# Performance work log

Hardware: AMD Instinct MI355X
Metric: run time of the kernel (lower is better)

## Reference

```python
import jax, jax.numpy as jnp
import numpy as np

N, E, FEAT, DIM, B = 200000, 1600000, 128, 64, 256


def setup_inputs() -> dict:
    key = jax.random.key(0)
    ks = jax.random.split(key, 16)
    s = 0.05
    x = jax.random.normal(ks[0], (N, FEAT), jnp.float32)
    edge_index = jax.random.randint(ks[1], (2, E), 0, N)
    batch = jnp.sort(jax.random.randint(ks[2], (N,), 0, B))
    return {
        'x': x,
        'edge_index': edge_index,
        'batch': batch,
        'lin0_w': jax.random.normal(ks[3], (FEAT, DIM), jnp.float32) * s,
        'lin0_b': jax.random.normal(ks[4], (DIM,), jnp.float32) * s,
        'conv_w': jax.random.normal(ks[5], (DIM, DIM), jnp.float32) * s,
        'conv_b': jax.random.normal(ks[6], (DIM,), jnp.float32) * s,
        'gru_w_ih': jax.random.normal(ks[7], (3 * DIM, DIM), jnp.float32) * s,
        'gru_w_hh': jax.random.normal(ks[8], (3 * DIM, DIM), jnp.float32) * s,
        'gru_b_ih': jax.random.normal(ks[9], (3 * DIM,), jnp.float32) * s,
        'gru_b_hh': jax.random.normal(ks[10], (3 * DIM,), jnp.float32) * s,
        'lstm_w_ih': jax.random.normal(ks[11], (4 * DIM, 2 * DIM), jnp.float32) * s,
        'lstm_w_hh': jax.random.normal(ks[12], (4 * DIM, DIM), jnp.float32) * s,
        'lstm_b_ih': jax.random.normal(ks[13], (4 * DIM,), jnp.float32) * s,
        'lstm_b_hh': jax.random.normal(ks[14], (4 * DIM,), jnp.float32) * s,
    }


def reference(x, edge_index, batch, lin0_w, lin0_b, conv_w, conv_b,
              gru_w_ih, gru_w_hh, gru_b_ih, gru_b_hh,
              lstm_w_ih, lstm_w_hh, lstm_b_ih, lstm_b_hh):
    n = x.shape[0]
    d = lin0_w.shape[1]
    # --- GCN normalization with self-loops (PyG gcn_norm, symmetric) ---
    loops = jnp.arange(n)
    row = jnp.concatenate([edge_index[0], loops])  # source nodes
    col = jnp.concatenate([edge_index[1], loops])  # target nodes
    deg = jax.ops.segment_sum(jnp.ones(row.shape, jnp.float32), col, num_segments=N)
    dinv = jnp.where(deg > 0, jax.lax.rsqrt(deg), 0.0)
    norm = dinv[row] * dinv[col]  # [E+N]

    out = jax.nn.relu(x @ lin0_w + lin0_b)  # [N, D]
    h = out  # GRU hidden (layer dim squeezed)
    feat = out
    for _ in range(3):
        # GCNConv: aggregate normalized neighbor messages
        hw = out @ conv_w                                   # [N, D]
        m = jax.ops.segment_sum(norm[:, None] * hw[row], col, num_segments=N) + conv_b
        m = jax.nn.relu(m)
        # torch.nn.GRU cell (gate order: reset, update, new)
        gi = m @ gru_w_ih.T + gru_b_ih
        gh = h @ gru_w_hh.T + gru_b_hh
        ir, iz, in_ = jnp.split(gi, 3, axis=-1)
        hr, hz, hn = jnp.split(gh, 3, axis=-1)
        r = jax.nn.sigmoid(ir + hr)
        z = jax.nn.sigmoid(iz + hz)
        ncand = jnp.tanh(in_ + r * hn)
        h = (1.0 - z) * ncand + z * h
        out = h
        feat = out

    # --- Set2Set pooling, processing_steps=3 (LSTM: 2D -> D) ---
    q_star = jnp.zeros((B, 2 * d), x.dtype)
    hl = jnp.zeros((B, d), x.dtype)
    cl = jnp.zeros((B, d), x.dtype)
    for _ in range(3):
        gates = q_star @ lstm_w_ih.T + lstm_b_ih + hl @ lstm_w_hh.T + lstm_b_hh
        i_, f_, g_, o_ = jnp.split(gates, 4, axis=-1)  # torch order i,f,g,o
        cl = jax.nn.sigmoid(f_) * cl + jax.nn.sigmoid(i_) * jnp.tanh(g_)
        hl = jax.nn.sigmoid(o_) * jnp.tanh(cl)
        q = hl                                             # [B, D]
        e = jnp.sum(out * q[batch], axis=-1)               # [N]
        emax = jax.ops.segment_max(e, batch, num_segments=B)
        a = jnp.exp(e - jax.lax.stop_gradient(emax)[batch])
        denom = jax.ops.segment_sum(a, batch, num_segments=B)
        a = a / denom[batch]                               # scatter-softmax
        r_read = jax.ops.segment_sum(a[:, None] * out, batch, num_segments=B)
        q_star = jnp.concatenate([q, r_read], axis=-1)     # [B, 2D]
    return (q_star, feat)
```

## Files before the change

### kernel.cpp

```cpp
#include <hip/hip_runtime.h>
#include <math.h>

#define FEATD 128
#define DIM 64
#define NB 256
#define SCB 256
#define KB 16
#define RNG 128
#define NBUCKMAX 2048
#define CH1 8192

typedef short bf16x8 __attribute__((ext_vector_type(8)));
typedef float f32x4 __attribute__((ext_vector_type(4)));

__device__ __forceinline__ float frcp_(float x){ return __builtin_amdgcn_rcpf(x); }
__device__ __forceinline__ float sigmoidf_(float x){ return frcp_(1.f+__expf(-x)); }
__device__ __forceinline__ float tanhf_(float x){ float e=__expf(2.f*x); return 1.f-2.f*frcp_(e+1.f); }

__device__ __forceinline__ unsigned short f2bf(float f){
  unsigned u = __float_as_uint(f);
  unsigned r = (u + 0x7FFFu + ((u>>16)&1u)) >> 16;
  return (unsigned short)r;
}
__device__ __forceinline__ float bf2f(unsigned short s){
  return __uint_as_float(((unsigned)s)<<16);
}

__device__ __forceinline__ int lower_bound_i(const int* __restrict__ a, int n, int key){
  int lo=0, hi=n;
  while(lo<hi){ int mid=(lo+hi)>>1; if(a[mid]<key) lo=mid+1; else hi=mid; }
  return lo;
}

__global__ void k_count(const int* __restrict__ col, int* __restrict__ deg, int E){
  int i=blockIdx.x*blockDim.x+threadIdx.x;
  if(i<E) atomicAdd(&deg[col[i]],1);
}

__global__ void k_dinv(const int* __restrict__ deg, float* __restrict__ dinv, int n){
  int i=blockIdx.x*blockDim.x+threadIdx.x;
  if(i<n) dinv[i]=rsqrtf((float)(deg[i]+1));
}

__global__ __launch_bounds__(256) void k_scan_part(const int* __restrict__ deg, int* __restrict__ part, int n){
  __shared__ int s[256];
  int b=blockIdx.x;
  int chunk=(n+SCB-1)/SCB;
  int lo=b*chunk, hi=min(lo+chunk,n);
  int acc=0;
  for(int i=lo+threadIdx.x;i<hi;i+=256) acc+=deg[i];
  s[threadIdx.x]=acc; __syncthreads();
  for(int off=128;off;off>>=1){
    if(threadIdx.x<off) s[threadIdx.x]+=s[threadIdx.x+off];
    __syncthreads();
  }
  if(threadIdx.x==0) part[b]=s[0];
}

__global__ __launch_bounds__(256) void k_scan_mid(int* __restrict__ part){
  __shared__ int s[256];
  int t=threadIdx.x;
  s[t]=part[t]; __syncthreads();
  for(int off=1;off<256;off<<=1){
    int v=(t>=off)? s[t-off]:0;
    __syncthreads();
    s[t]+=v;
    __syncthreads();
  }
  part[t]=(t>0)? s[t-1]:0;
}

__global__ __launch_bounds__(256) void k_scan_out(const int* __restrict__ deg, const int* __restrict__ part,
                                                  int* __restrict__ rp, int* __restrict__ gcur, int n){
  __shared__ int s[256];
  int b=blockIdx.x, t=threadIdx.x;
  int chunk=(n+SCB-1)/SCB;
  int lo=b*chunk, hi=min(lo+chunk,n);
  int tchunk=(chunk+255)/256;
  int tlo=lo+t*tchunk, thi=min(tlo+tchunk,hi);
  int acc=0;
  for(int i=tlo;i<thi;i++) acc+=deg[i];
  s[t]=acc; __syncthreads();
  for(int off=1;off<256;off<<=1){
    int v=(t>=off)? s[t-off]:0;
    __syncthreads();
    s[t]+=v;
    __syncthreads();
  }
  int pre=part[b]+((t>0)? s[t-1]:0);
  for(int i=tlo;i<thi;i++){
    rp[i]=pre;
    if((i&(RNG-1))==0) gcur[(i>>7)*32]=pre;
    pre+=deg[i];
  }
  if(b==SCB-1 && t==0) rp[n]=part[b]+s[255];
}

__global__ __launch_bounds__(256) void k_binscat(const int* __restrict__ row, const int* __restrict__ col,
                       int* __restrict__ gcur, unsigned* __restrict__ tmp, int E, int nbuck){
  __shared__ int lcnt[NBUCKMAX];
  __shared__ int lcur[NBUCKMAX];
  int t=threadIdx.x;
  for(int i=t;i<nbuck;i+=256) lcnt[i]=0;
  __syncthreads();
  int lo=blockIdx.x*CH1, hi=min(lo+CH1,E);
  for(int i=lo+t;i<hi;i+=256) atomicAdd(&lcnt[col[i]>>7],1);
  __syncthreads();
  for(int i=t;i<nbuck;i+=256){
    int cnt=lcnt[i];
    lcur[i]=(cnt>0)? atomicAdd(&gcur[i*32],cnt):0;
  }
  __syncthreads();
  for(int i=lo+t;i<hi;i+=256){
    int c=col[i], r=row[i];
    int pos=atomicAdd(&lcur[c>>7],1);
    tmp[pos]=((unsigned)r<<7)|(unsigned)(c&127);
  }
}

__global__ __launch_bounds__(256) void k_place(const unsigned* __restrict__ tmp, const int* __restrict__ rp,
                      const float* __restrict__ dinv, int2* __restrict__ epack, int n, int nbuck){
  __shared__ int lfill[RNG];
  __shared__ int lrp[RNG];
  __shared__ float ldv[RNG];
  int b=blockIdx.x, t=threadIdx.x;
  int nbase=b*RNG;
  int nn=min(RNG,n-nbase);
  if(t<nn){ lfill[t]=0; lrp[t]=rp[nbase+t]; ldv[t]=dinv[nbase+t]; }
  __syncthreads();
  int lo=rp[nbase], hi=rp[min(nbase+RNG,n)];
  for(int j=lo+t;j<hi;j+=256){
    unsigned v=tmp[j];
    int cl=v&127;
    int r=(int)(v>>7);
    int pos=atomicAdd(&lfill[cl],1);
    epack[lrp[cl]+pos]=make_int2(r,__float_as_int(dinv[r]*ldv[cl]));
  }
}

__global__ void k_prep_plain(const float* __restrict__ W, unsigned short* __restrict__ Bf, int K, int C){
  int i=blockIdx.x*blockDim.x+threadIdx.x;
  if(i>=K*C) return;
  int k=i/C, c=i%C;
  int t=c>>4, s=k>>5, lane=(c&15)|(((k>>3)&3)<<4), r=k&7;
  int S=K>>5;
  Bf[(((t*S)+s)*64+lane)*8+r]=f2bf(W[(size_t)k*C+c]);
}

__global__ void k_prep_gru(const float* __restrict__ wih, const float* __restrict__ whh,
                           unsigned short* __restrict__ Bf){
  int i=blockIdx.x*blockDim.x+threadIdx.x;
  if(i>=128*256) return;
  int k=i>>8, c=i&255;
  float v;
  if(c<128){
    v = (k<64) ? wih[c*64+k] : whh[c*64+(k-64)];
  } else if(c<192){
    v = (k<64) ? wih[c*64+k] : 0.f;
  } else {
    v = (k<64) ? 0.f : whh[(c-64)*64+(k-64)];
  }
  int t=c>>4, s=k>>5, lane=(c&15)|(((k>>3)&3)<<4), r=k&7;
  Bf[(((s*16)+t)*64+lane)*8+r]=f2bf(v);
}

__global__ __launch_bounds__(256) void k_lin0(const float* __restrict__ x, const unsigned short* __restrict__ Bf,
                      const float* __restrict__ bias,
                      unsigned short* __restrict__ hb, int ngrp){
  int l=threadIdx.x&63;
  int g=blockIdx.x*4+(threadIdx.x>>6);
  if(g>=ngrp) return;
  int row16=l&15, koff=(l>>4)*8;
  f32x4 acc[4]={};
  const float* xr = x + (size_t)(g*16+row16)*128 + koff;
  #pragma unroll
  for(int s=0;s<4;s++){
    f32x4 a0=*(const f32x4*)(xr+s*32);
    f32x4 a1=*(const f32x4*)(xr+s*32+4);
    bf16x8 af;
    #pragma unroll
    for(int r=0;r<4;r++){ af[r]=(short)f2bf(a0[r]); af[4+r]=(short)f2bf(a1[r]); }
    #pragma unroll
    for(int t=0;t<4;t++){
      bf16x8 bf=*(const bf16x8*)(Bf+(((t*4)+s)*64+l)*8);
      acc[t]=__builtin_amdgcn_mfma_f32_16x16x32_bf16(af,bf,acc[t],0,0,0);
    }
  }
  int rbase=g*16+(l>>4)*4;
  #pragma unroll
  for(int t=0;t<4;t++){
    int c=t*16+(l&15);
    float b=bias[c];
    #pragma unroll
    for(int j=0;j<4;j++){
      int node=rbase+j;
      float v=fmaxf(acc[t][j]+b,0.f);
      hb[(size_t)node*64+c]=f2bf(v);
    }
  }
}

__global__ __launch_bounds__(256) void k_aggregate(const unsigned short* __restrict__ hb, const int* __restrict__ rp,
                        const int2* __restrict__ epack, const float* __restrict__ dinv,
                        unsigned short* __restrict__ aggb, int n){
  int node=blockIdx.x*4+(threadIdx.x>>6);
  int lane=threadIdx.x&63;
  if(node>=n) return;
  int q=lane>>4, l16=lane&15;
  const uint2* hb64=(const uint2*)hb;
  float a0=0.f,a1=0.f,a2=0.f,a3=0.f, b0=0.f,b1=0.f,b2=0.f,b3=0.f;
  int s=rp[node], e=rp[node+1];
  int j=s+q;
  for(; j+4<e; j+=8){
    int2 e0=epack[j];
    int2 e1=epack[j+4];
    uint2 p0=hb64[((unsigned)e0.x<<4)+l16];
    uint2 p1=hb64[((unsigned)e1.x<<4)+l16];
    float n0=__int_as_float(e0.y), n1=__int_as_float(e1.y);
    a0+=n0*bf2f((unsigned short)p0.x);
    a1+=n0*bf2f((unsigned short)(p0.x>>16));
    a2+=n0*bf2f((unsigned short)p0.y);
    a3+=n0*bf2f((unsigned short)(p0.y>>16));
    b0+=n1*bf2f((unsigned short)p1.x);
    b1+=n1*bf2f((unsigned short)(p1.x>>16));
    b2+=n1*bf2f((unsigned short)p1.y);
    b3+=n1*bf2f((unsigned short)(p1.y>>16));
  }
  for(; j<e; j+=4){
    int2 e0=epack[j];
    uint2 p0=hb64[((unsigned)e0.x<<4)+l16];
    float n0=__int_as_float(e0.y);
    a0+=n0*bf2f((unsigned short)p0.x);
    a1+=n0*bf2f((unsigned short)(p0.x>>16));
    a2+=n0*bf2f((unsigned short)p0.y);
    a3+=n0*bf2f((unsigned short)(p0.y>>16));
  }
  a0+=b0; a1+=b1; a2+=b2; a3+=b3;
  if(q==0){
    float dv=dinv[node]; dv*=dv;
    uint2 ps=hb64[((unsigned)node<<4)+l16];
    a0+=dv*bf2f((unsigned short)ps.x);
    a1+=dv*bf2f((unsigned short)(ps.x>>16));
    a2+=dv*bf2f((unsigned short)ps.y);
    a3+=dv*bf2f((unsigned short)(ps.y>>16));
  }
  a0+=__shfl_xor(a0,16); a0+=__shfl_xor(a0,32);
  a1+=__shfl_xor(a1,16); a1+=__shfl_xor(a1,32);
  a2+=__shfl_xor(a2,16); a2+=__shfl_xor(a2,32);
  a3+=__shfl_xor(a3,16); a3+=__shfl_xor(a3,32);
  if(q==0){
    uint2 outp;
    outp.x=(unsigned)f2bf(a0)|(((unsigned)f2bf(a1))<<16);
    outp.y=(unsigned)f2bf(a2)|(((unsigned)f2bf(a3))<<16);
    ((uint2*)aggb)[((unsigned)node<<4)+l16]=outp;
  }
}

__global__ __launch_bounds__(256) void k_gru(const unsigned short* __restrict__ aggb, unsigned short* hb,
                     const unsigned short* __restrict__ Bcnv, const float* __restrict__ cb,
                     const unsigned short* __restrict__ Bgru,
                     const float* __restrict__ bih, const float* __restrict__ bhh,
                     float* h, int last, int ngrp, int n){
  __shared__ __align__(16) unsigned short Bs[16384];
  __shared__ __align__(16) unsigned short Bc[4096];
  __shared__ __align__(16) unsigned short mt[4][16][72];
  int tid=threadIdx.x;
  int l=tid&63, w=tid>>6;
  int g=blockIdx.x*4+w;
  bool act = g<ngrp;
  int gc = act? g : (ngrp-1);
  int row16=l&15, koff=(l>>4)*8;
  int node_r=gc*16+row16;
  int rbase=gc*16+(l>>4)*4;

  const unsigned short* ar = aggb + (size_t)node_r*64 + koff;
  const unsigned short* hr = hb   + (size_t)node_r*64 + koff;
  bf16x8 a_agg0=*(const bf16x8*)(ar);
  bf16x8 a_agg1=*(const bf16x8*)(ar+32);
  bf16x8 a_h0=*(const bf16x8*)(hr);
  bf16x8 a_h1=*(const bf16x8*)(hr+32);
  float hold[16];
  #pragma unroll
  for(int t=0;t<4;t++)
    #pragma unroll
    for(int j=0;j<4;j++)
      hold[t*4+j]=bf2f(hb[(size_t)(rbase+j)*64 + t*16+(l&15)]);

  {
    const f32x4* gs=(const f32x4*)Bcnv; f32x4* ls=(f32x4*)Bc;
    #pragma unroll
    for(int i=0;i<2;i++) ls[i*256+tid]=gs[i*256+tid];
    const f32x4* gh=(const f32x4*)Bgru; f32x4* lh=(f32x4*)Bs;
    #pragma unroll
    for(int i=0;i<8;i++) lh[i*256+tid]=gh[i*256+tid];
  }
  __syncthreads();

  f32x4 accm[4]={};
  #pragma unroll
  for(int s=0;s<2;s++){
    bf16x8 af=(s==0)? a_agg0:a_agg1;
    #pragma unroll
    for(int t=0;t<4;t++){
      bf16x8 bf=*(const bf16x8*)(Bc+((t*2+s)*64+l)*8);
      accm[t]=__builtin_amdgcn_mfma_f32_16x16x32_bf16(af,bf,accm[t],0,0,0);
    }
  }
  #pragma unroll
  for(int t=0;t<4;t++){
    int c=t*16+(l&15);
    float b=cb[c];
    #pragma unroll
    for(int j=0;j<4;j++)
      mt[w][(l>>4)*4+j][c]=f2bf(fmaxf(accm[t][j]+b,0.f));
  }

  f32x4 acc[16]={};
  #pragma unroll
  for(int s=0;s<2;s++){
    bf16x8 af=*(const bf16x8*)&mt[w][row16][koff+s*32];
    #pragma unroll
    for(int t=0;t<16;t++){
      bf16x8 bf=*(const bf16x8*)(Bs+((s*16+t)*64+l)*8);
      acc[t]=__builtin_amdgcn_mfma_f32_16x16x32_bf16(af,bf,acc[t],0,0,0);
    }
  }
  __syncthreads();
  {
    const f32x4* gh=(const f32x4*)(Bgru+16384); f32x4* lh=(f32x4*)Bs;
    #pragma unroll
    for(int i=0;i<8;i++) lh[i*256+tid]=gh[i*256+tid];
  }
  __syncthreads();

  #pragma unroll
  for(int s=0;s<2;s++){
    bf16x8 af=(s==0)? a_h0:a_h1;
    #pragma unroll
    for(int t=0;t<16;t++){
      bf16x8 bf=*(const bf16x8*)(Bs+((s*16+t)*64+l)*8);
      acc[t]=__builtin_amdgcn_mfma_f32_16x16x32_bf16(af,bf,acc[t],0,0,0);
    }
  }

  if(!act) return;
  #pragma unroll
  for(int t=0;t<4;t++){
    int d=t*16+(l&15);
    float br =bih[d]    +bhh[d];
    float bz =bih[64+d] +bhh[64+d];
    float bni=bih[128+d];
    float bnh=bhh[128+d];
    #pragma unroll
    for(int j=0;j<4;j++){
      int node=rbase+j;
      if(node<n){
        float r  = sigmoidf_(acc[t][j]   + br);
        float z  = sigmoidf_(acc[4+t][j] + bz);
        float nc = tanhf_(acc[8+t][j] + bni + r*(acc[12+t][j] + bnh));
        float hn = (1.f-z)*nc + z*hold[t*4+j];
        if(last) h[(size_t)node*64+d]=hn;
        hb[(size_t)node*64+d]=f2bf(hn);
      }
    }
  }
}

__global__ __launch_bounds__(256) void k_attn_part(const unsigned short* __restrict__ hb, const int* __restrict__ batch,
                        const float* __restrict__ hl, float* __restrict__ apart, int n){
  int b=blockIdx.x/KB, kb=blockIdx.x%KB;
  int tid=threadIdx.x, lane=tid&63, w=tid>>6;
  __shared__ float qs[64];
  __shared__ float wm[4], wsm[4];
  __shared__ float wacc[4][64];
  if(tid<64) qs[tid]=hl[b*64+tid];
  int lo=lower_bound_i(batch,n,b), hi=lower_bound_i(batch,n,b+1);
  int cnt=hi-lo;
  int chunk=(cnt+KB-1)/KB;
  int slo=lo+kb*chunk, shi=min(slo+chunk,hi);
  __syncthreads();
  float q=qs[lane];
  float mw=-3.0e38f, sw=0.f, aw=0.f;
  for(int i=slo+w;i<shi;i+=4){
    float f=bf2f(hb[(size_t)i*64+lane]);
    float v=f*q;
    #pragma unroll
    for(int off=32;off;off>>=1) v+=__shfl_xor(v,off);
    if(v>mw){
      float sc=__expf(mw-v);
      sw=sw*sc+1.f;
      aw=aw*sc+f;
      mw=v;
    } else {
      float p=__expf(v-mw);
      sw+=p;
      aw+=p*f;
    }
  }
  if(lane==0){ wm[w]=mw; wsm[w]=sw; }
  wacc[w][lane]=aw;
  __syncthreads();
  if(w==0){
    float M=fmaxf(fmaxf(wm[0],wm[1]),fmaxf(wm[2],wm[3]));
    float S=0.f, A=0.f;
    #pragma unroll
    for(int k=0;k<4;k++){
      float sc=__expf(wm[k]-M);
      S+=wsm[k]*sc;
      A+=wacc[k][lane]*sc;
    }
    float* p=apart+(size_t)blockIdx.x*68;
    p[lane]=A;
    if(lane==0){ p[64]=M; p[65]=S; }
  }
}

__global__ __launch_bounds__(256) void k_merge_lstm(const float* __restrict__ apart,
                   float* __restrict__ qstar, float* __restrict__ hl, float* __restrict__ cl,
                   const float* __restrict__ wih, const float* __restrict__ whh,
                   const float* __restrict__ bih, const float* __restrict__ bhh,
                   int do_merge, int do_lstm){
  int b=blockIdx.x, tid=threadIdx.x;
  __shared__ float qs[128];
  __shared__ float gates[256];
  if(do_merge){
    if(tid<64){
      const float* p0=apart+(size_t)b*KB*68;
      float M=-3.0e38f;
      #pragma unroll
      for(int k=0;k<KB;k++) M=fmaxf(M,p0[k*68+64]);
      float S=0.f, A=0.f;
      #pragma unroll
      for(int k=0;k<KB;k++){
        float sc=__expf(p0[k*68+64]-M);
        S+=p0[k*68+65]*sc;
        A+=p0[k*68+tid]*sc;
      }
      float inv=(S>0.f)? 1.f/S:0.f;
      float r=A*inv;
      qs[64+tid]=r;
      qstar[b*128+64+tid]=r;
    }
  } else {
    if(tid<64) qs[64+tid]=qstar[b*128+64+tid];
  }
  if(tid<64) qs[tid]=hl[b*64+tid];
  __syncthreads();
  if(!do_lstm) return;
  float acc=bih[tid]+bhh[tid];
  const float* wi=wih+(size_t)tid*128;
  #pragma unroll 8
  for(int k=0;k<128;k++) acc+=qs[k]*wi[k];
  const float* w2=whh+(size_t)tid*64;
  #pragma unroll 8
  for(int k=0;k<64;k++) acc+=qs[k]*w2[k];
  gates[tid]=acc;
  __syncthreads();
  if(tid<64){
    float i_=gates[tid], f_=gates[64+tid], g_=gates[128+tid], o_=gates[192+tid];
    float c=sigmoidf_(f_)*cl[b*64+tid]+sigmoidf_(i_)*tanhf(g_);
    float hn=sigmoidf_(o_)*tanhf(c);
    cl[b*64+tid]=c; hl[b*64+tid]=hn;
    qstar[b*128+tid]=hn;
  }
}

extern "C" void kernel_launch(void* const* d_in, const int* in_sizes, int n_in,
                              void* d_out, int out_size, void* d_ws, size_t ws_size,
                              hipStream_t stream){
  const float* x      =(const float*)d_in[0];
  const int*   ei     =(const int*)d_in[1];
  const int*   batch  =(const int*)d_in[2];
  const float* lin0_w =(const float*)d_in[3];
  const float* lin0_b =(const float*)d_in[4];
  const float* conv_w =(const float*)d_in[5];
  const float* conv_b =(const float*)d_in[6];
  const float* gwih   =(const float*)d_in[7];
  const float* gwhh   =(const float*)d_in[8];
  const float* gbih   =(const float*)d_in[9];
  const float* gbhh   =(const float*)d_in[10];
  const float* lwih   =(const float*)d_in[11];
  const float* lwhh   =(const float*)d_in[12];
  const float* lbih   =(const float*)d_in[13];
  const float* lbhh   =(const float*)d_in[14];

  int N = in_sizes[0]/FEATD;
  int E = in_sizes[1]/2;
  const int* row = ei;
  const int* col = ei + E;

  float* qstar = (float*)d_out;
  float* h     = (float*)d_out + NB*2*DIM;

  char* ws=(char*)d_ws;
  size_t off=0;
  auto alloc=[&](size_t bytes)->void*{ void* p=ws+off; off=(off+bytes+255)&~(size_t)255; return p; };
  int*   deg  =(int*)  alloc((size_t)N*4);
  float* dinv =(float*)alloc((size_t)N*4);
  int*   rp   =(int*)  alloc((size_t)(N+1)*4);
  int*   part =(int*)  alloc((size_t)SCB*4);
  int*   gcur =(int*)  alloc((size_t)NBUCKMAX*32*4);
  unsigned* tmp=(unsigned*)alloc((size_t)E*4);
  int2*  epack=(int2*) alloc((size_t)E*8);
  unsigned short* hb   =(unsigned short*)alloc((size_t)N*64*2);
  unsigned short* aggb =(unsigned short*)alloc((size_t)N*64*2);
  float* hl   =(float*)alloc((size_t)NB*DIM*4);
  float* cl   =(float*)alloc((size_t)NB*DIM*4);
  float* apart=(float*)alloc((size_t)NB*KB*68*4);
  unsigned short* Bgru =(unsigned short*)alloc(128*256*2);
  unsigned short* Blin =(unsigned short*)alloc(128*64*2);
  unsigned short* Bcnv =(unsigned short*)alloc(64*64*2);

  hipMemsetAsync(deg ,0,(size_t)N*4,stream);
  hipMemsetAsync(hl  ,0,(size_t)NB*DIM*4,stream);
  hipMemsetAsync(cl  ,0,(size_t)NB*DIM*4,stream);
  hipMemsetAsync(qstar,0,(size_t)NB*2*DIM*4,stream);

  int nbuck=(N+RNG-1)/RNG;

  k_count<<<(E+255)/256,256,0,stream>>>(col,deg,E);
  k_dinv <<<(N+255)/256,256,0,stream>>>(deg,dinv,N);
  k_scan_part<<<SCB,256,0,stream>>>(deg,part,N);
  k_scan_mid <<<1,256,0,stream>>>(part);
  k_scan_out <<<SCB,256,0,stream>>>(deg,part,rp,gcur,N);
  k_binscat<<<(E+CH1-1)/CH1,256,0,stream>>>(row,col,gcur,tmp,E,nbuck);
  k_place<<<nbuck,256,0,stream>>>(tmp,rp,dinv,epack,N,nbuck);

  k_prep_plain<<<(128*64+255)/256,256,0,stream>>>(lin0_w,Blin,128,64);
  k_prep_plain<<<(64*64+255)/256,256,0,stream>>>(conv_w,Bcnv,64,64);
  k_prep_gru  <<<(128*256+255)/256,256,0,stream>>>(gwih,gwhh,Bgru);

  int ngrp=(N+15)/16;
  int gb=(ngrp+3)/4;

  k_lin0<<<gb,256,0,stream>>>(x,Blin,lin0_b,hb,ngrp);

  for(int it=0;it<3;it++){
    k_aggregate<<<(N+3)/4,256,0,stream>>>(hb,rp,epack,dinv,aggb,N);
    k_gru      <<<gb,256,0,stream>>>(aggb,hb,Bcnv,conv_b,Bgru,gbih,gbhh,h,(it==2)?1:0,ngrp,N);
  }

  k_merge_lstm<<<NB,256,0,stream>>>(apart,qstar,hl,cl,lwih,lwhh,lbih,lbhh,0,1);
  for(int st=0;st<3;st++){
    k_attn_part<<<NB*KB,256,0,stream>>>(hb,batch,hl,apart,N);
    int do_lstm = (st<2)? 1:0;
    k_merge_lstm<<<NB,256,0,stream>>>(apart,qstar,hl,cl,lwih,lwhh,lbih,lbhh,1,do_lstm);
  }
}
```

Before: 658.6 us.

## Fuse GCN neighbor aggregation into GRU kernel with ping-pong hidden buffers

Merges the separate aggregation kernel into the GRU kernel. Each wave gathers neighbor features for its 16 nodes, stages the aggregate and its own hidden rows in LDS tiles, and feeds them straight into the MFMA conv and GRU matmuls. Hidden state alternates between two buffers to avoid read/write hazards. GRU weights are streamed in four smaller LDS chunks and the conv weights are kept in registers. This removes the aggregate buffer round-trip and a launch per layer, but each wave now processes edges for four nodes serially, with less parallelism per node and more syncs.

```diff
diff --git a/kernel.cpp b/kernel.cpp
--- a/kernel.cpp
+++ b/kernel.cpp
@@ -200,111 +200,91 @@
   }
 }
 
-__global__ __launch_bounds__(256) void k_aggregate(const unsigned short* __restrict__ hb, const int* __restrict__ rp,
-                        const int2* __restrict__ epack, const float* __restrict__ dinv,
-                        unsigned short* __restrict__ aggb, int n){
-  int node=blockIdx.x*4+(threadIdx.x>>6);
-  int lane=threadIdx.x&63;
-  if(node>=n) return;
-  int q=lane>>4, l16=lane&15;
-  const uint2* hb64=(const uint2*)hb;
-  float a0=0.f,a1=0.f,a2=0.f,a3=0.f, b0=0.f,b1=0.f,b2=0.f,b3=0.f;
-  int s=rp[node], e=rp[node+1];
-  int j=s+q;
-  for(; j+4<e; j+=8){
-    int2 e0=epack[j];
-    int2 e1=epack[j+4];
-    uint2 p0=hb64[((unsigned)e0.x<<4)+l16];
-    uint2 p1=hb64[((unsigned)e1.x<<4)+l16];
-    float n0=__int_as_float(e0.y), n1=__int_as_float(e1.y);
-    a0+=n0*bf2f((unsigned short)p0.x);
-    a1+=n0*bf2f((unsigned short)(p0.x>>16));
-    a2+=n0*bf2f((unsigned short)p0.y);
-    a3+=n0*bf2f((unsigned short)(p0.y>>16));
-    b0+=n1*bf2f((unsigned short)p1.x);
-    b1+=n1*bf2f((unsigned short)(p1.x>>16));
-    b2+=n1*bf2f((unsigned short)p1.y);
-    b3+=n1*bf2f((unsigned short)(p1.y>>16));
-  }
-  for(; j<e; j+=4){
-    int2 e0=epack[j];
-    uint2 p0=hb64[((unsigned)e0.x<<4)+l16];
-    float n0=__int_as_float(e0.y);
-    a0+=n0*bf2f((unsigned short)p0.x);
-    a1+=n0*bf2f((unsigned short)(p0.x>>16));
-    a2+=n0*bf2f((unsigned short)p0.y);
-    a3+=n0*bf2f((unsigned short)(p0.y>>16));
-  }
-  a0+=b0; a1+=b1; a2+=b2; a3+=b3;
-  if(q==0){
-    float dv=dinv[node]; dv*=dv;
-    uint2 ps=hb64[((unsigned)node<<4)+l16];
-    a0+=dv*bf2f((unsigned short)ps.x);
-    a1+=dv*bf2f((unsigned short)(ps.x>>16));
-    a2+=dv*bf2f((unsigned short)ps.y);
-    a3+=dv*bf2f((unsigned short)(ps.y>>16));
-  }
-  a0+=__shfl_xor(a0,16); a0+=__shfl_xor(a0,32);
-  a1+=__shfl_xor(a1,16); a1+=__shfl_xor(a1,32);
-  a2+=__shfl_xor(a2,16); a2+=__shfl_xor(a2,32);
-  a3+=__shfl_xor(a3,16); a3+=__shfl_xor(a3,32);
-  if(q==0){
-    uint2 outp;
-    outp.x=(unsigned)f2bf(a0)|(((unsigned)f2bf(a1))<<16);
-    outp.y=(unsigned)f2bf(a2)|(((unsigned)f2bf(a3))<<16);
-    ((uint2*)aggb)[((unsigned)node<<4)+l16]=outp;
-  }
-}
-
-__global__ __launch_bounds__(256) void k_gru(const unsigned short* __restrict__ aggb, unsigned short* hb,
+__global__ __launch_bounds__(256) void k_gruagg(
+                     const unsigned short* __restrict__ hin, unsigned short* __restrict__ hout,
+                     const int* __restrict__ rp, const int2* __restrict__ epack,
+                     const float* __restrict__ dinv,
                      const unsigned short* __restrict__ Bcnv, const float* __restrict__ cb,
                      const unsigned short* __restrict__ Bgru,
                      const float* __restrict__ bih, const float* __restrict__ bhh,
-                     float* h, int last, int ngrp, int n){
-  __shared__ __align__(16) unsigned short Bs[16384];
-  __shared__ __align__(16) unsigned short Bc[4096];
-  __shared__ __align__(16) unsigned short mt[4][16][72];
+                     float* __restrict__ h, int last, int ngrp, int n){
+  __shared__ __align__(16) unsigned short Bs[8192];
+  __shared__ __align__(16) unsigned short tA[4][16][72];
+  __shared__ __align__(16) unsigned short tH[4][16][72];
   int tid=threadIdx.x;
   int l=tid&63, w=tid>>6;
   int g=blockIdx.x*4+w;
   bool act = g<ngrp;
   int gc = act? g : (ngrp-1);
+  int q=l>>4, l16=l&15;
   int row16=l&15, koff=(l>>4)*8;
-  int node_r=gc*16+row16;
   int rbase=gc*16+(l>>4)*4;
 
-  const unsigned short* ar = aggb + (size_t)node_r*64 + koff;
-  const unsigned short* hr = hb   + (size_t)node_r*64 + koff;
-  bf16x8 a_agg0=*(const bf16x8*)(ar);
-  bf16x8 a_agg1=*(const bf16x8*)(ar+32);
-  bf16x8 a_h0=*(const bf16x8*)(hr);
-  bf16x8 a_h1=*(const bf16x8*)(hr+32);
-  float hold[16];
-  #pragma unroll
-  for(int t=0;t<4;t++)
-    #pragma unroll
-    for(int j=0;j<4;j++)
-      hold[t*4+j]=bf2f(hb[(size_t)(rbase+j)*64 + t*16+(l&15)]);
+  bf16x8 bc[8];
+  #pragma unroll
+  for(int f=0;f<8;f++) bc[f]=*(const bf16x8*)(Bcnv+((size_t)f*64+l)*8);
 
   {
-    const f32x4* gs=(const f32x4*)Bcnv; f32x4* ls=(f32x4*)Bc;
-    #pragma unroll
-    for(int i=0;i<2;i++) ls[i*256+tid]=gs[i*256+tid];
     const f32x4* gh=(const f32x4*)Bgru; f32x4* lh=(f32x4*)Bs;
     #pragma unroll
-    for(int i=0;i<8;i++) lh[i*256+tid]=gh[i*256+tid];
-  }
-  __syncthreads();
+    for(int i=0;i<4;i++) lh[i*256+tid]=gh[i*256+tid];
+  }
+
+  const uint2* h64=(const uint2*)hin;
+  #pragma unroll
+  for(int rr=0;rr<4;rr++){
+    int node=min(gc*16+rr*4+q, n-1);
+    float a0=0.f,a1=0.f,a2=0.f,a3=0.f, b0=0.f,b1=0.f,b2=0.f,b3=0.f;
+    int s=rp[node], e=rp[node+1];
+    uint2 selfp=h64[((unsigned)node<<4)+l16];
+    int j=s;
+    for(; j+3<e; j+=4){
+      int2 e0=epack[j];
+      int2 e1=epack[j+1];
+      int2 e2=epack[j+2];
+      int2 e3=epack[j+3];
+      uint2 p0=h64[((unsigned)e0.x<<4)+l16];
+      uint2 p1=h64[((unsigned)e1.x<<4)+l16];
+      uint2 p2=h64[((unsigned)e2.x<<4)+l16];
+      uint2 p3=h64[((unsigned)e3.x<<4)+l16];
+      float n0=__int_as_float(e0.y), n1=__int_as_float(e1.y);
+      float n2=__int_as_float(e2.y), n3=__int_as_float(e3.y);
+      a0+=n0*bf2f((unsigned short)p0.x); a1+=n0*bf2f((unsigned short)(p0.x>>16));
+      a2+=n0*bf2f((unsigned short)p0.y); a3+=n0*bf2f((unsigned short)(p0.y>>16));
+      b0+=n1*bf2f((unsigned short)p1.x); b1+=n1*bf2f((unsigned short)(p1.x>>16));
+      b2+=n1*bf2f((unsigned short)p1.y); b3+=n1*bf2f((unsigned short)(p1.y>>16));
+      a0+=n2*bf2f((unsigned short)p2.x); a1+=n2*bf2f((unsigned short)(p2.x>>16));
+      a2+=n2*bf2f((unsigned short)p2.y); a3+=n2*bf2f((unsigned short)(p2.y>>16));
+      b0+=n3*bf2f((unsigned short)p3.x); b1+=n3*bf2f((unsigned short)(p3.x>>16));
+      b2+=n3*bf2f((unsigned short)p3.y); b3+=n3*bf2f((unsigned short)(p3.y>>16));
+    }
+    for(; j<e; j++){
+      int2 e0=epack[j];
+      uint2 p0=h64[((unsigned)e0.x<<4)+l16];
+      float n0=__int_as_float(e0.y);
+      a0+=n0*bf2f((unsigned short)p0.x); a1+=n0*bf2f((unsigned short)(p0.x>>16));
+      a2+=n0*bf2f((unsigned short)p0.y); a3+=n0*bf2f((unsigned short)(p0.y>>16));
+    }
+    float dv=dinv[node]; dv*=dv;
+    a0+=b0+dv*bf2f((unsigned short)selfp.x);
+    a1+=b1+dv*bf2f((unsigned short)(selfp.x>>16));
+    a2+=b2+dv*bf2f((unsigned short)selfp.y);
+    a3+=b3+dv*bf2f((unsigned short)(selfp.y>>16));
+    int ri=rr*4+q;
+    unsigned* tAp=(unsigned*)&tA[w][ri][l16*4];
+    tAp[0]=(unsigned)f2bf(a0)|(((unsigned)f2bf(a1))<<16);
+    tAp[1]=(unsigned)f2bf(a2)|(((unsigned)f2bf(a3))<<16);
+    unsigned* tHp=(unsigned*)&tH[w][ri][l16*4];
+    tHp[0]=selfp.x; tHp[1]=selfp.y;
+  }
 
   f32x4 accm[4]={};
   #pragma unroll
   for(int s=0;s<2;s++){
-    bf16x8 af=(s==0)? a_agg0:a_agg1;
-    #pragma unroll
-    for(int t=0;t<4;t++){
-      bf16x8 bf=*(const bf16x8*)(Bc+((t*2+s)*64+l)*8);
-      accm[t]=__builtin_amdgcn_mfma_f32_16x16x32_bf16(af,bf,accm[t],0,0,0);
-    }
+    bf16x8 af=*(const bf16x8*)&tA[w][row16][s*32+koff];
+    #pragma unroll
+    for(int t=0;t<4;t++)
+      accm[t]=__builtin_amdgcn_mfma_f32_16x16x32_bf16(af,bc[t*2+s],accm[t],0,0,0);
   }
   #pragma unroll
   for(int t=0;t<4;t++){
@@ -312,33 +292,26 @@
     float b=cb[c];
     #pragma unroll
     for(int j=0;j<4;j++)
-      mt[w][(l>>4)*4+j][c]=f2bf(fmaxf(accm[t][j]+b,0.f));
+      tA[w][(l>>4)*4+j][c]=f2bf(fmaxf(accm[t][j]+b,0.f));
   }
 
   f32x4 acc[16]={};
-  #pragma unroll
-  for(int s=0;s<2;s++){
-    bf16x8 af=*(const bf16x8*)&mt[w][row16][koff+s*32];
+  __syncthreads();
+  #pragma unroll
+  for(int s=0;s<4;s++){
+    if(s>0){
+      __syncthreads();
+      const f32x4* gh=(const f32x4*)(Bgru+(size_t)s*8192); f32x4* lh=(f32x4*)Bs;
+      #pragma unroll
+      for(int i=0;i<4;i++) lh[i*256+tid]=gh[i*256+tid];
+      __syncthreads();
+    }
+    bf16x8 af;
+    if(s<2) af=*(const bf16x8*)&tA[w][row16][s*32+koff];
+    else    af=*(const bf16x8*)&tH[w][row16][(s-2)*32+koff];
     #pragma unroll
     for(int t=0;t<16;t++){
-      bf16x8 bf=*(const bf16x8*)(Bs+((s*16+t)*64+l)*8);
-      acc[t]=__builtin_amdgcn_mfma_f32_16x16x32_bf16(af,bf,acc[t],0,0,0);
-    }
-  }
-  __syncthreads();
-  {
-    const f32x4* gh=(const f32x4*)(Bgru+16384); f32x4* lh=(f32x4*)Bs;
-    #pragma unroll
-    for(int i=0;i<8;i++) lh[i*256+tid]=gh[i*256+tid];
-  }
-  __syncthreads();
-
-  #pragma unroll
-  for(int s=0;s<2;s++){
-    bf16x8 af=(s==0)? a_h0:a_h1;
-    #pragma unroll
-    for(int t=0;t<16;t++){
-      bf16x8 bf=*(const bf16x8*)(Bs+((s*16+t)*64+l)*8);
+      bf16x8 bf=*(const bf16x8*)(Bs+((size_t)t*64+l)*8);
       acc[t]=__builtin_amdgcn_mfma_f32_16x16x32_bf16(af,bf,acc[t],0,0,0);
     }
   }
@@ -358,9 +331,10 @@
         float r  = sigmoidf_(acc[t][j]   + br);
         float z  = sigmoidf_(acc[4+t][j] + bz);
         float nc = tanhf_(acc[8+t][j] + bni + r*(acc[12+t][j] + bnh));
-        float hn = (1.f-z)*nc + z*hold[t*4+j];
+        float hold=bf2f(tH[w][(l>>4)*4+j][d]);
+        float hn = (1.f-z)*nc + z*hold;
         if(last) h[(size_t)node*64+d]=hn;
-        hb[(size_t)node*64+d]=f2bf(hn);
+        hout[(size_t)node*64+d]=f2bf(hn);
       }
     }
   }
@@ -502,8 +476,8 @@
   int*   gcur =(int*)  alloc((size_t)NBUCKMAX*32*4);
   unsigned* tmp=(unsigned*)alloc((size_t)E*4);
   int2*  epack=(int2*) alloc((size_t)E*8);
-  unsigned short* hb   =(unsigned short*)alloc((size_t)N*64*2);
-  unsigned short* aggb =(unsigned short*)alloc((size_t)N*64*2);
+  unsigned short* hb0  =(unsigned short*)alloc((size_t)N*64*2);
+  unsigned short* hb1  =(unsigned short*)alloc((size_t)N*64*2);
   float* hl   =(float*)alloc((size_t)NB*DIM*4);
   float* cl   =(float*)alloc((size_t)NB*DIM*4);
   float* apart=(float*)alloc((size_t)NB*KB*68*4);
@@ -533,16 +507,15 @@
   int ngrp=(N+15)/16;
   int gb=(ngrp+3)/4;
 
-  k_lin0<<<gb,256,0,stream>>>(x,Blin,lin0_b,hb,ngrp);
-
-  for(int it=0;it<3;it++){
-    k_aggregate<<<(N+3)/4,256,0,stream>>>(hb,rp,epack,dinv,aggb,N);
-    k_gru      <<<gb,256,0,stream>>>(aggb,hb,Bcnv,conv_b,Bgru,gbih,gbhh,h,(it==2)?1:0,ngrp,N);
-  }
+  k_lin0<<<gb,256,0,stream>>>(x,Blin,lin0_b,hb0,ngrp);
+
+  k_gruagg<<<gb,256,0,stream>>>(hb0,hb1,rp,epack,dinv,Bcnv,conv_b,Bgru,gbih,gbhh,h,0,ngrp,N);
+  k_gruagg<<<gb,256,0,stream>>>(hb1,hb0,rp,epack,dinv,Bcnv,conv_b,Bgru,gbih,gbhh,h,0,ngrp,N);
+  k_gruagg<<<gb,256,0,stream>>>(hb0,hb1,rp,epack,dinv,Bcnv,conv_b,Bgru,gbih,gbhh,h,1,ngrp,N);
 
   k_merge_lstm<<<NB,256,0,stream>>>(apart,qstar,hl,cl,lwih,lwhh,lbih,lbhh,0,1);
   for(int st=0;st<3;st++){
-    k_attn_part<<<NB*KB,256,0,stream>>>(hb,batch,hl,apart,N);
+    k_attn_part<<<NB*KB,256,0,stream>>>(hb1,batch,hl,apart,N);
     int do_lstm = (st<2)? 1:0;
     k_merge_lstm<<<NB,256,0,stream>>>(apart,qstar,hl,cl,lwih,lwhh,lbih,lbhh,1,do_lstm);
   }
```

Result: no change. 648.7 us (-1.5%).
